# Kernel tuning notes

Hardware: AMD Instinct MI355X
Metric: run time of the kernel (lower is better)

The kernel has to match this reference:

```python
import jax, jax.numpy as jnp
import numpy as np

N_IN = 512    # samples per input window
N_VP = 12     # number of weighted Hermite basis functions
BATCH = 65536


def ada_weighted_hermite(n_in, n_vp, params):
    """Adaptive weighted Hermite system (VPNet-style).

    params = [dilation, translation].
    Returns phi [n_in, n_vp], dphi [n_in, 2*n_vp] (d/d dilation cols then
    d/d translation cols), ind [2, 2*n_vp] (row 0: basis index, row 1: param index).
    """
    dilation, translation = params[0], params[1]
    t = jnp.arange(n_in, dtype=params.dtype) - (n_in - 1) / 2.0  # centered grid
    xs = dilation * (t - translation)  # [n_in]
    pi14 = jnp.pi ** -0.25
    phi0 = pi14 * jnp.exp(-0.5 * xs * xs)
    phis = [phi0]
    if n_vp > 1:
        phis.append(jnp.sqrt(2.0) * xs * phi0)
    for k in range(2, n_vp):
        phis.append(jnp.sqrt(2.0 / k) * xs * phis[k - 1]
                    - jnp.sqrt((k - 1) / k) * phis[k - 2])
    phi = jnp.stack(phis, axis=1)  # [n_in, n_vp]
    # d phi_k / d xs = sqrt(2k) phi_{k-1} - xs * phi_k
    dphis = [-xs * phis[0]]
    for k in range(1, n_vp):
        dphis.append(jnp.sqrt(2.0 * k) * phis[k - 1] - xs * phis[k])
    dphi_dx = jnp.stack(dphis, axis=1)  # [n_in, n_vp]
    d_dil = dphi_dx * (t - translation)[:, None]   # chain rule: dxs/d dilation
    d_tr = -dilation * dphi_dx                     # dxs/d translation
    dphi = jnp.concatenate([d_dil, d_tr], axis=1)  # [n_in, 2*n_vp]
    ind = jnp.stack([jnp.tile(jnp.arange(n_vp), 2),
                     jnp.repeat(jnp.arange(2), n_vp)])  # [2, 2*n_vp]
    return phi, dphi, ind


def setup_inputs() -> dict:
    key = jax.random.key(0)
    kx, _ = jax.random.split(key)
    x = jax.random.normal(kx, (BATCH, N_IN), dtype=jnp.float32)
    w = jnp.array([0.1, 0.0], dtype=jnp.float32)  # [dilation, translation]
    return {"x": x, "w": w}


def reference(x, w):
    phi, dphi, ind = ada_weighted_hermite(N_IN, N_VP, w)
    phip = jnp.linalg.pinv(phi, rcond=1e-15)      # [n_vp, n_in]
    coeffs = phip @ x.T                           # [n_vp, batch]
    return coeffs.T                               # [batch, n_vp]
```

## Files before the change

kernel.cpp:

```cpp
#include <hip/hip_runtime.h>

#define N_IN 512
#define N_VP 12
#define BATCH 65536

#define SPLIT 4
#define ROWS 64
#define CPW (N_IN / SPLIT)
#define CHUNK 16
#define NCHW (CPW / CHUNK)

__global__ __launch_bounds__(512) void build_W_kernel(const float* __restrict__ w,
                                                      float* __restrict__ Wg) {
    __shared__ float sphiT[N_VP][N_IN];
    __shared__ float Gp[2][N_VP][N_VP];
    __shared__ float G[N_VP][N_VP], Y[N_VP][N_VP], T[N_VP][N_VP];

    const int tid = threadIdx.x;
    const float dil = w[0];
    const float tr  = w[1];

    float ph[N_VP];
    {
        const float t  = (float)tid - 0.5f * (float)(N_IN - 1);
        const float xs = dil * (t - tr);
        ph[0] = 0.7511255444649425f * expf(-0.5f * xs * xs);
        ph[1] = 1.4142135623730951f * xs * ph[0];
#pragma unroll
        for (int k = 2; k < N_VP; ++k)
            ph[k] = sqrtf(2.0f / (float)k) * xs * ph[k - 1]
                  - sqrtf((float)(k - 1) / (float)k) * ph[k - 2];
#pragma unroll
        for (int k = 0; k < N_VP; ++k) sphiT[k][tid] = ph[k];
    }
    __syncthreads();

    if (tid < 288) {
        const int p = tid >> 1;
        const int i = p / N_VP, j = p % N_VP;
        const int m0 = (tid & 1) * 256;
        const float4* __restrict__ pi = reinterpret_cast<const float4*>(&sphiT[i][m0]);
        const float4* __restrict__ pj = reinterpret_cast<const float4*>(&sphiT[j][m0]);
        float s = 0.0f;
#pragma unroll 4
        for (int q = 0; q < 64; ++q) {
            const float4 a = pi[q], b = pj[q];
            s += a.x * b.x + a.y * b.y + a.z * b.z + a.w * b.w;
        }
        Gp[tid & 1][i][j] = s;
    }
    __syncthreads();
    const int ii = (tid < 144) ? tid / N_VP : 0;
    const int jj = (tid < 144) ? tid % N_VP : 0;
    if (tid < 144) {
        G[ii][jj] = Gp[0][ii][jj] + Gp[1][ii][jj];
        Y[ii][jj] = (ii == jj) ? dil : 0.0f;
    }
    __syncthreads();

    for (int it = 0; it < 3; ++it) {
        if (tid < 144) {
            float s = 0.0f;
#pragma unroll
            for (int k = 0; k < N_VP; ++k) s += G[ii][k] * Y[k][jj];
            T[ii][jj] = s;
        }
        __syncthreads();
        float v = 0.0f;
        if (tid < 144) {
            float s = 0.0f;
#pragma unroll
            for (int k = 0; k < N_VP; ++k) s += Y[ii][k] * T[k][jj];
            v = 2.0f * Y[ii][jj] - s;
        }
        __syncthreads();
        if (tid < 144) Y[ii][jj] = v;
        __syncthreads();
    }

#pragma unroll
    for (int k = 0; k < N_VP; ++k) {
        float s = 0.0f;
#pragma unroll
        for (int j2 = 0; j2 < N_VP; ++j2) s += Y[k][j2] * ph[j2];
        Wg[tid * N_VP + k] = s;
    }
}

__device__ __forceinline__ void load_chunk(const float* __restrict__ xq,
                                           const int off[4], int c, float4 pre[4]) {
#pragma unroll
    for (int i = 0; i < 4; ++i)
        pre[i] = *reinterpret_cast<const float4*>(xq + off[i] + c * CHUNK);
}

__device__ __forceinline__ void store_chunk(float4* __restrict__ dst, int lane,
                                            const float4 pre[4]) {
#pragma unroll
    for (int i = 0; i < 4; ++i) dst[i * 64 + lane] = pre[i];
}

__device__ __forceinline__ void compute_chunk(const float4* __restrict__ buf,
                                              int lane, int qx,
                                              const float* __restrict__ wb,
                                              float acc[N_VP]) {
#pragma unroll
    for (int q = 0; q < 4; ++q) {
        const float4 xv = buf[(lane << 2) + (q ^ qx)];
        const float* __restrict__ w4 = wb + q * (4 * N_VP);
#pragma unroll
        for (int k = 0; k < N_VP; ++k) acc[k] = fmaf(xv.x, w4[k], acc[k]);
#pragma unroll
        for (int k = 0; k < N_VP; ++k) acc[k] = fmaf(xv.y, w4[N_VP + k], acc[k]);
#pragma unroll
        for (int k = 0; k < N_VP; ++k) acc[k] = fmaf(xv.z, w4[2 * N_VP + k], acc[k]);
#pragma unroll
        for (int k = 0; k < N_VP; ++k) acc[k] = fmaf(xv.w, w4[3 * N_VP + k], acc[k]);
    }
}

__global__ __launch_bounds__(256, 4) void coeffs_kernel(const float* __restrict__ x,
                                                        const float* __restrict__ Wg,
                                                        float* __restrict__ out) {
    __shared__ float4 sb[SPLIT][2][256];
    const int tid  = threadIdx.x;
    const int lane = tid & 63;
    const int s    = __builtin_amdgcn_readfirstlane(tid >> 6);
    const int qx   = (lane >> 1) & 3;
    const size_t rowbase = (size_t)blockIdx.x * ROWS;
    const float* __restrict__ xq = x + rowbase * N_IN + (size_t)s * CPW;
    const float* __restrict__ wbase = Wg + s * CPW * N_VP;

    int off[4];
#pragma unroll
    for (int i = 0; i < 4; ++i) {
        const int f = i * 64 + lane, t = f >> 2, q0 = f & 3;
        const int qg = q0 ^ ((t >> 1) & 3);
        off[i] = t * N_IN + qg * 4;
    }

    float4 preA[4], preB[4];
    load_chunk(xq, off, 0, preA);
    load_chunk(xq, off, 1, preB);
    store_chunk(&sb[s][0][0], lane, preA);

    float acc[N_VP];
#pragma unroll
    for (int k = 0; k < N_VP; ++k) acc[k] = 0.0f;

#pragma unroll
    for (int c = 0; c < NCHW; ++c) {
        if (c + 1 < NCHW) store_chunk(&sb[s][(c + 1) & 1][0], lane,
                                      (c & 1) ? preA : preB);
        if (c + 2 < NCHW) load_chunk(xq, off, c + 2,
                                     (c & 1) ? preB : preA);
        compute_chunk(&sb[s][c & 1][0], lane, qx, wbase + c * (CHUNK * N_VP), acc);
    }

    __syncthreads();
    float4* part4 = reinterpret_cast<float4*>(&sb[0][0][0]);
    part4[s * 192 + lane * 3 + 0] = make_float4(acc[0], acc[1], acc[2],  acc[3]);
    part4[s * 192 + lane * 3 + 1] = make_float4(acc[4], acc[5], acc[6],  acc[7]);
    part4[s * 192 + lane * 3 + 2] = make_float4(acc[8], acc[9], acc[10], acc[11]);
    __syncthreads();
    if (tid < 192) {
        const float4 v0 = part4[tid], v1 = part4[192 + tid];
        const float4 v2 = part4[384 + tid], v3 = part4[576 + tid];
        float4 r;
        r.x = (v0.x + v1.x) + (v2.x + v3.x);
        r.y = (v0.y + v1.y) + (v2.y + v3.y);
        r.z = (v0.z + v1.z) + (v2.z + v3.z);
        r.w = (v0.w + v1.w) + (v2.w + v3.w);
        reinterpret_cast<float4*>(out + rowbase * N_VP)[tid] = r;
    }
}

extern "C" void kernel_launch(void* const* d_in, const int* in_sizes, int n_in,
                              void* d_out, int out_size, void* d_ws, size_t ws_size,
                              hipStream_t stream) {
    const float* x  = (const float*)d_in[0];
    const float* w  = (const float*)d_in[1];
    float* out      = (float*)d_out;
    float* Wg       = (float*)d_ws;

    build_W_kernel<<<1, 512, 0, stream>>>(w, Wg);
    coeffs_kernel<<<BATCH / ROWS, 256, 0, stream>>>(x, Wg, out);
}
```

Before: 42.88 us.

## Stream x chunks directly into LDS with global_load_lds and manual waitcnt

Replaces the register-staged double buffer (global load into VGPRs, then LDS store) with asynchronous global_load_lds transfers that write straight into shared memory. Explicit vmcnt and lgkmcnt waits plus sched_barriers order each chunk's arrival, its read into registers, and the issue of the chunk two steps ahead. The occupancy hint of 4 blocks per CU is also dropped from launch_bounds. This removes the staging VGPRs and the LDS store instructions, but relies on hand-counted wait counts, which are fragile if the compiler emits other memory operations such as the W loads.

```diff
diff --git a/kernel.cpp b/kernel.cpp
--- a/kernel.cpp
+++ b/kernel.cpp
@@ -9,6 +9,9 @@
 #define CPW (N_IN / SPLIT)
 #define CHUNK 16
 #define NCHW (CPW / CHUNK)
+
+#define GLB_CAST(p) ((const __attribute__((address_space(1))) unsigned int*)(p))
+#define LDS_CAST(p) ((__attribute__((address_space(3))) unsigned int*)(p))
 
 __global__ __launch_bounds__(512) void build_W_kernel(const float* __restrict__ w,
                                                       float* __restrict__ Wg) {
@@ -87,41 +90,9 @@
     }
 }
 
-__device__ __forceinline__ void load_chunk(const float* __restrict__ xq,
-                                           const int off[4], int c, float4 pre[4]) {
-#pragma unroll
-    for (int i = 0; i < 4; ++i)
-        pre[i] = *reinterpret_cast<const float4*>(xq + off[i] + c * CHUNK);
-}
-
-__device__ __forceinline__ void store_chunk(float4* __restrict__ dst, int lane,
-                                            const float4 pre[4]) {
-#pragma unroll
-    for (int i = 0; i < 4; ++i) dst[i * 64 + lane] = pre[i];
-}
-
-__device__ __forceinline__ void compute_chunk(const float4* __restrict__ buf,
-                                              int lane, int qx,
-                                              const float* __restrict__ wb,
-                                              float acc[N_VP]) {
-#pragma unroll
-    for (int q = 0; q < 4; ++q) {
-        const float4 xv = buf[(lane << 2) + (q ^ qx)];
-        const float* __restrict__ w4 = wb + q * (4 * N_VP);
-#pragma unroll
-        for (int k = 0; k < N_VP; ++k) acc[k] = fmaf(xv.x, w4[k], acc[k]);
-#pragma unroll
-        for (int k = 0; k < N_VP; ++k) acc[k] = fmaf(xv.y, w4[N_VP + k], acc[k]);
-#pragma unroll
-        for (int k = 0; k < N_VP; ++k) acc[k] = fmaf(xv.z, w4[2 * N_VP + k], acc[k]);
-#pragma unroll
-        for (int k = 0; k < N_VP; ++k) acc[k] = fmaf(xv.w, w4[3 * N_VP + k], acc[k]);
-    }
-}
-
-__global__ __launch_bounds__(256, 4) void coeffs_kernel(const float* __restrict__ x,
-                                                        const float* __restrict__ Wg,
-                                                        float* __restrict__ out) {
+__global__ __launch_bounds__(256) void coeffs_kernel(const float* __restrict__ x,
+                                                     const float* __restrict__ Wg,
+                                                     float* __restrict__ out) {
     __shared__ float4 sb[SPLIT][2][256];
     const int tid  = threadIdx.x;
     const int lane = tid & 63;
@@ -139,10 +110,17 @@
         off[i] = t * N_IN + qg * 4;
     }
 
-    float4 preA[4], preB[4];
-    load_chunk(xq, off, 0, preA);
-    load_chunk(xq, off, 1, preB);
-    store_chunk(&sb[s][0][0], lane, preA);
+#define ISSUE_CHUNK(c)                                                         \
+    {                                                                          \
+        float4* dst_ = &sb[s][(c) & 1][0];                                     \
+        _Pragma("unroll")                                                      \
+        for (int i_ = 0; i_ < 4; ++i_)                                         \
+            __builtin_amdgcn_global_load_lds(GLB_CAST(xq + off[i_] + (c) * CHUNK), \
+                                             LDS_CAST(dst_ + i_ * 64), 16, 0, 0); \
+    }
+
+    ISSUE_CHUNK(0)
+    ISSUE_CHUNK(1)
 
     float acc[N_VP];
 #pragma unroll
@@ -150,11 +128,32 @@
 
 #pragma unroll
     for (int c = 0; c < NCHW; ++c) {
-        if (c + 1 < NCHW) store_chunk(&sb[s][(c + 1) & 1][0], lane,
-                                      (c & 1) ? preA : preB);
-        if (c + 2 < NCHW) load_chunk(xq, off, c + 2,
-                                     (c & 1) ? preB : preA);
-        compute_chunk(&sb[s][c & 1][0], lane, qx, wbase + c * (CHUNK * N_VP), acc);
+        if (c < NCHW - 1) asm volatile("s_waitcnt vmcnt(4)" ::: "memory");
+        else              asm volatile("s_waitcnt vmcnt(0)" ::: "memory");
+        __builtin_amdgcn_sched_barrier(0);
+
+        const float4* __restrict__ buf = &sb[s][c & 1][0];
+        float4 xv[4];
+#pragma unroll
+        for (int q = 0; q < 4; ++q) xv[q] = buf[(lane << 2) + (q ^ qx)];
+
+        asm volatile("s_waitcnt lgkmcnt(0)" ::: "memory");
+        __builtin_amdgcn_sched_barrier(0);
+        if (c + 2 < NCHW) ISSUE_CHUNK(c + 2)
+
+        const float* __restrict__ wb = wbase + c * (CHUNK * N_VP);
+#pragma unroll
+        for (int q = 0; q < 4; ++q) {
+            const float* __restrict__ w4 = wb + q * (4 * N_VP);
+#pragma unroll
+            for (int k = 0; k < N_VP; ++k) acc[k] = fmaf(xv[q].x, w4[k], acc[k]);
+#pragma unroll
+            for (int k = 0; k < N_VP; ++k) acc[k] = fmaf(xv[q].y, w4[N_VP + k], acc[k]);
+#pragma unroll
+            for (int k = 0; k < N_VP; ++k) acc[k] = fmaf(xv[q].z, w4[2 * N_VP + k], acc[k]);
+#pragma unroll
+            for (int k = 0; k < N_VP; ++k) acc[k] = fmaf(xv[q].w, w4[3 * N_VP + k], acc[k]);
+        }
     }
 
     __syncthreads();
```

Result: slower. 46.77 us (+9.1%).

## Widen coalesced row loads and use single swizzled LDS buffer per wave

Applied to the files above, without the earlier changes.

Doubles the per-wave chunk width to 32 floats. Each row is now fetched by 8 lanes as a contiguous 128-byte segment, where before 4 lanes fetched 64 bytes. The per-wave double-buffered LDS staging is replaced by one XOR-swizzled row-major buffer, written after the compute on the current chunk, with two register prefetch sets of 8 float4 each. The aim is better global-memory coalescing and fewer load instructions per byte on this bandwidth-bound projection. The cost is higher register pressure and a serialized compute-then-store order inside each wave.

```diff
diff --git a/kernel.cpp b/kernel.cpp
--- a/kernel.cpp
+++ b/kernel.cpp
@@ -4,10 +4,10 @@
 #define N_VP 12
 #define BATCH 65536
 
-#define SPLIT 4
+#define WAVES 4
 #define ROWS 64
-#define CPW (N_IN / SPLIT)
-#define CHUNK 16
+#define CPW (N_IN / WAVES)
+#define CHUNK 32
 #define NCHW (CPW / CHUNK)
 
 __global__ __launch_bounds__(512) void build_W_kernel(const float* __restrict__ w,
@@ -87,62 +87,44 @@
     }
 }
 
-__device__ __forceinline__ void load_chunk(const float* __restrict__ xq,
-                                           const int off[4], int c, float4 pre[4]) {
-#pragma unroll
-    for (int i = 0; i < 4; ++i)
-        pre[i] = *reinterpret_cast<const float4*>(xq + off[i] + c * CHUNK);
-}
-
-__device__ __forceinline__ void store_chunk(float4* __restrict__ dst, int lane,
-                                            const float4 pre[4]) {
-#pragma unroll
-    for (int i = 0; i < 4; ++i) dst[i * 64 + lane] = pre[i];
-}
-
-__device__ __forceinline__ void compute_chunk(const float4* __restrict__ buf,
-                                              int lane, int qx,
-                                              const float* __restrict__ wb,
-                                              float acc[N_VP]) {
-#pragma unroll
-    for (int q = 0; q < 4; ++q) {
-        const float4 xv = buf[(lane << 2) + (q ^ qx)];
-        const float* __restrict__ w4 = wb + q * (4 * N_VP);
-#pragma unroll
-        for (int k = 0; k < N_VP; ++k) acc[k] = fmaf(xv.x, w4[k], acc[k]);
-#pragma unroll
-        for (int k = 0; k < N_VP; ++k) acc[k] = fmaf(xv.y, w4[N_VP + k], acc[k]);
-#pragma unroll
-        for (int k = 0; k < N_VP; ++k) acc[k] = fmaf(xv.z, w4[2 * N_VP + k], acc[k]);
-#pragma unroll
-        for (int k = 0; k < N_VP; ++k) acc[k] = fmaf(xv.w, w4[3 * N_VP + k], acc[k]);
-    }
-}
-
 __global__ __launch_bounds__(256, 4) void coeffs_kernel(const float* __restrict__ x,
                                                         const float* __restrict__ Wg,
                                                         float* __restrict__ out) {
-    __shared__ float4 sb[SPLIT][2][256];
+    __shared__ float sb[WAVES][ROWS][CHUNK];
     const int tid  = threadIdx.x;
     const int lane = tid & 63;
     const int s    = __builtin_amdgcn_readfirstlane(tid >> 6);
-    const int qx   = (lane >> 1) & 3;
     const size_t rowbase = (size_t)blockIdx.x * ROWS;
-    const float* __restrict__ xq = x + rowbase * N_IN + (size_t)s * CPW;
+    const float* __restrict__ xq = x + rowbase * N_IN + s * CPW;
     const float* __restrict__ wbase = Wg + s * CPW * N_VP;
 
-    int off[4];
+    const int t0 = lane >> 3, q0 = lane & 7;
+    const int gbase = t0 * N_IN + q0 * 4;
+    float* const wr0 = &sb[s][0][0] + t0 * CHUNK + ((q0 ^ (t0 & 7)) << 2);
+
+    const float* rd[8];
 #pragma unroll
-    for (int i = 0; i < 4; ++i) {
-        const int f = i * 64 + lane, t = f >> 2, q0 = f & 3;
-        const int qg = q0 ^ ((t >> 1) & 3);
-        off[i] = t * N_IN + qg * 4;
+    for (int g = 0; g < 8; ++g)
+        rd[g] = &sb[s][lane][(g ^ (lane & 7)) << 2];
+
+#define LOADC(c, pre)                                                          \
+    {                                                                          \
+        _Pragma("unroll")                                                      \
+        for (int i_ = 0; i_ < 8; ++i_)                                         \
+            pre[i_] = *reinterpret_cast<const float4*>(                        \
+                xq + gbase + i_ * 8 * N_IN + (c) * CHUNK);                     \
+    }
+#define STOREC(pre)                                                            \
+    {                                                                          \
+        _Pragma("unroll")                                                      \
+        for (int i_ = 0; i_ < 8; ++i_)                                         \
+            *reinterpret_cast<float4*>(wr0 + i_ * 8 * CHUNK) = pre[i_];        \
     }
 
-    float4 preA[4], preB[4];
-    load_chunk(xq, off, 0, preA);
-    load_chunk(xq, off, 1, preB);
-    store_chunk(&sb[s][0][0], lane, preA);
+    float4 preA[8], preB[8];
+    LOADC(0, preA)
+    STOREC(preA)
+    LOADC(1, preB)
 
     float acc[N_VP];
 #pragma unroll
@@ -150,11 +132,26 @@
 
 #pragma unroll
     for (int c = 0; c < NCHW; ++c) {
-        if (c + 1 < NCHW) store_chunk(&sb[s][(c + 1) & 1][0], lane,
-                                      (c & 1) ? preA : preB);
-        if (c + 2 < NCHW) load_chunk(xq, off, c + 2,
-                                     (c & 1) ? preB : preA);
-        compute_chunk(&sb[s][c & 1][0], lane, qx, wbase + c * (CHUNK * N_VP), acc);
+        const float* __restrict__ wc = wbase + c * (CHUNK * N_VP);
+#pragma unroll
+        for (int g = 0; g < 8; ++g) {
+            const float4 xv = *reinterpret_cast<const float4*>(rd[g]);
+            const float* __restrict__ w4 = wc + g * (4 * N_VP);
+#pragma unroll
+            for (int k = 0; k < N_VP; ++k) acc[k] = fmaf(xv.x, w4[k], acc[k]);
+#pragma unroll
+            for (int k = 0; k < N_VP; ++k) acc[k] = fmaf(xv.y, w4[N_VP + k], acc[k]);
+#pragma unroll
+            for (int k = 0; k < N_VP; ++k) acc[k] = fmaf(xv.z, w4[2 * N_VP + k], acc[k]);
+#pragma unroll
+            for (int k = 0; k < N_VP; ++k) acc[k] = fmaf(xv.w, w4[3 * N_VP + k], acc[k]);
+        }
+        if (c + 1 < NCHW) {
+            if (c & 1) { STOREC(preA) } else { STOREC(preB) }
+        }
+        if (c + 2 < NCHW) {
+            if (c & 1) { LOADC(c + 2, preB) } else { LOADC(c + 2, preA) }
+        }
     }
 
     __syncthreads();
```

Result: no change. 43.45 us (+1.3%).

## Fuse projection-matrix build into coeffs kernel, computing W per block in LDS

Applied to the files above, without the earlier changes.

Removes the separate single-block build_W kernel and has each of the 1024 blocks recompute the Hermite basis, a symmetric Gram matrix (only the upper triangle), three Newton-Schulz iterations and the projection matrix W in LDS, before the streaming GEMV. This drops one kernel launch and the serial dependency on a one-block kernel, and W is read from LDS instead of global memory. The cost is redundant per-block setup with several syncthreads, 24KB of extra LDS per block that may lower occupancy, and a simpler single-buffered staging pipeline for x.

```diff
diff --git a/kernel.cpp b/kernel.cpp
--- a/kernel.cpp
+++ b/kernel.cpp
@@ -4,132 +4,24 @@
 #define N_VP 12
 #define BATCH 65536
 
-#define SPLIT 4
+#define WAVES 4
 #define ROWS 64
-#define CPW (N_IN / SPLIT)
+#define CPW (N_IN / WAVES)
 #define CHUNK 16
 #define NCHW (CPW / CHUNK)
 
-__global__ __launch_bounds__(512) void build_W_kernel(const float* __restrict__ w,
-                                                      float* __restrict__ Wg) {
-    __shared__ float sphiT[N_VP][N_IN];
-    __shared__ float Gp[2][N_VP][N_VP];
-    __shared__ float G[N_VP][N_VP], Y[N_VP][N_VP], T[N_VP][N_VP];
+__global__ __launch_bounds__(256, 4) void vp_fused_kernel(const float* __restrict__ x,
+                                                          const float* __restrict__ w,
+                                                          float* __restrict__ out) {
+    __shared__ float wlds[N_IN * N_VP];
+    __shared__ float stage[WAVES * ROWS * CHUNK];
 
-    const int tid = threadIdx.x;
-    const float dil = w[0];
-    const float tr  = w[1];
-
-    float ph[N_VP];
-    {
-        const float t  = (float)tid - 0.5f * (float)(N_IN - 1);
-        const float xs = dil * (t - tr);
-        ph[0] = 0.7511255444649425f * expf(-0.5f * xs * xs);
-        ph[1] = 1.4142135623730951f * xs * ph[0];
-#pragma unroll
-        for (int k = 2; k < N_VP; ++k)
-            ph[k] = sqrtf(2.0f / (float)k) * xs * ph[k - 1]
-                  - sqrtf((float)(k - 1) / (float)k) * ph[k - 2];
-#pragma unroll
-        for (int k = 0; k < N_VP; ++k) sphiT[k][tid] = ph[k];
-    }
-    __syncthreads();
-
-    if (tid < 288) {
-        const int p = tid >> 1;
-        const int i = p / N_VP, j = p % N_VP;
-        const int m0 = (tid & 1) * 256;
-        const float4* __restrict__ pi = reinterpret_cast<const float4*>(&sphiT[i][m0]);
-        const float4* __restrict__ pj = reinterpret_cast<const float4*>(&sphiT[j][m0]);
-        float s = 0.0f;
-#pragma unroll 4
-        for (int q = 0; q < 64; ++q) {
-            const float4 a = pi[q], b = pj[q];
-            s += a.x * b.x + a.y * b.y + a.z * b.z + a.w * b.w;
-        }
-        Gp[tid & 1][i][j] = s;
-    }
-    __syncthreads();
-    const int ii = (tid < 144) ? tid / N_VP : 0;
-    const int jj = (tid < 144) ? tid % N_VP : 0;
-    if (tid < 144) {
-        G[ii][jj] = Gp[0][ii][jj] + Gp[1][ii][jj];
-        Y[ii][jj] = (ii == jj) ? dil : 0.0f;
-    }
-    __syncthreads();
-
-    for (int it = 0; it < 3; ++it) {
-        if (tid < 144) {
-            float s = 0.0f;
-#pragma unroll
-            for (int k = 0; k < N_VP; ++k) s += G[ii][k] * Y[k][jj];
-            T[ii][jj] = s;
-        }
-        __syncthreads();
-        float v = 0.0f;
-        if (tid < 144) {
-            float s = 0.0f;
-#pragma unroll
-            for (int k = 0; k < N_VP; ++k) s += Y[ii][k] * T[k][jj];
-            v = 2.0f * Y[ii][jj] - s;
-        }
-        __syncthreads();
-        if (tid < 144) Y[ii][jj] = v;
-        __syncthreads();
-    }
-
-#pragma unroll
-    for (int k = 0; k < N_VP; ++k) {
-        float s = 0.0f;
-#pragma unroll
-        for (int j2 = 0; j2 < N_VP; ++j2) s += Y[k][j2] * ph[j2];
-        Wg[tid * N_VP + k] = s;
-    }
-}
-
-__device__ __forceinline__ void load_chunk(const float* __restrict__ xq,
-                                           const int off[4], int c, float4 pre[4]) {
-#pragma unroll
-    for (int i = 0; i < 4; ++i)
-        pre[i] = *reinterpret_cast<const float4*>(xq + off[i] + c * CHUNK);
-}
-
-__device__ __forceinline__ void store_chunk(float4* __restrict__ dst, int lane,
-                                            const float4 pre[4]) {
-#pragma unroll
-    for (int i = 0; i < 4; ++i) dst[i * 64 + lane] = pre[i];
-}
-
-__device__ __forceinline__ void compute_chunk(const float4* __restrict__ buf,
-                                              int lane, int qx,
-                                              const float* __restrict__ wb,
-                                              float acc[N_VP]) {
-#pragma unroll
-    for (int q = 0; q < 4; ++q) {
-        const float4 xv = buf[(lane << 2) + (q ^ qx)];
-        const float* __restrict__ w4 = wb + q * (4 * N_VP);
-#pragma unroll
-        for (int k = 0; k < N_VP; ++k) acc[k] = fmaf(xv.x, w4[k], acc[k]);
-#pragma unroll
-        for (int k = 0; k < N_VP; ++k) acc[k] = fmaf(xv.y, w4[N_VP + k], acc[k]);
-#pragma unroll
-        for (int k = 0; k < N_VP; ++k) acc[k] = fmaf(xv.z, w4[2 * N_VP + k], acc[k]);
-#pragma unroll
-        for (int k = 0; k < N_VP; ++k) acc[k] = fmaf(xv.w, w4[3 * N_VP + k], acc[k]);
-    }
-}
-
-__global__ __launch_bounds__(256, 4) void coeffs_kernel(const float* __restrict__ x,
-                                                        const float* __restrict__ Wg,
-                                                        float* __restrict__ out) {
-    __shared__ float4 sb[SPLIT][2][256];
     const int tid  = threadIdx.x;
     const int lane = tid & 63;
     const int s    = __builtin_amdgcn_readfirstlane(tid >> 6);
     const int qx   = (lane >> 1) & 3;
     const size_t rowbase = (size_t)blockIdx.x * ROWS;
-    const float* __restrict__ xq = x + rowbase * N_IN + (size_t)s * CPW;
-    const float* __restrict__ wbase = Wg + s * CPW * N_VP;
+    const float* __restrict__ xq = x + rowbase * N_IN + s * CPW;
 
     int off[4];
 #pragma unroll
@@ -139,10 +31,113 @@
         off[i] = t * N_IN + qg * 4;
     }
 
-    float4 preA[4], preB[4];
-    load_chunk(xq, off, 0, preA);
-    load_chunk(xq, off, 1, preB);
-    store_chunk(&sb[s][0][0], lane, preA);
+    float4 pre[4];
+#pragma unroll
+    for (int i = 0; i < 4; ++i)
+        pre[i] = *reinterpret_cast<const float4*>(xq + off[i]);
+
+    const float dil = w[0];
+    const float tr  = w[1];
+
+#pragma unroll
+    for (int half = 0; half < 2; ++half) {
+        const int n = tid + half * 256;
+        const float t  = (float)n - 0.5f * (float)(N_IN - 1);
+        const float xs = dil * (t - tr);
+        float pm2 = 0.7511255444649425f * expf(-0.5f * xs * xs);
+        float pm1 = 1.4142135623730951f * xs * pm2;
+        wlds[0 * N_IN + n] = pm2;
+        wlds[1 * N_IN + n] = pm1;
+#pragma unroll
+        for (int k = 2; k < N_VP; ++k) {
+            const float pk = sqrtf(2.0f / (float)k) * xs * pm1
+                           - sqrtf((float)(k - 1) / (float)k) * pm2;
+            wlds[k * N_IN + n] = pk;
+            pm2 = pm1; pm1 = pk;
+        }
+    }
+    __syncthreads();
+
+    float* const Gp = stage;
+    float* const G  = stage + 160;
+    float* const Y  = stage + 304;
+    float* const T  = stage + 448;
+
+    if (tid < 156) {
+        const int p = tid >> 1, h = tid & 1;
+        int i = 0, rem = p;
+        while (rem >= N_VP - i) { rem -= N_VP - i; ++i; }
+        const int j = i + rem;
+        const float4* __restrict__ pi =
+            reinterpret_cast<const float4*>(wlds + i * N_IN + h * 256);
+        const float4* __restrict__ pj =
+            reinterpret_cast<const float4*>(wlds + j * N_IN + h * 256);
+        float acc = 0.0f;
+#pragma unroll 4
+        for (int q = 0; q < 64; ++q) {
+            const float4 a = pi[q], b = pj[q];
+            acc += a.x * b.x + a.y * b.y + a.z * b.z + a.w * b.w;
+        }
+        Gp[h * 78 + p] = acc;
+    }
+    __syncthreads();
+    if (tid < 78) {
+        int i = 0, rem = tid;
+        while (rem >= N_VP - i) { rem -= N_VP - i; ++i; }
+        const int j = i + rem;
+        const float v = Gp[tid] + Gp[78 + tid];
+        G[i * N_VP + j] = v;
+        G[j * N_VP + i] = v;
+    }
+    if (tid < 144) {
+        const int ii = tid / N_VP, jj = tid % N_VP;
+        Y[tid] = (ii == jj) ? dil : 0.0f;
+    }
+    __syncthreads();
+
+    for (int it = 0; it < 3; ++it) {
+        if (tid < 144) {
+            const int ii = tid / N_VP, jj = tid % N_VP;
+            float sa = 0.0f;
+#pragma unroll
+            for (int k = 0; k < N_VP; ++k) sa += G[ii * N_VP + k] * Y[k * N_VP + jj];
+            T[tid] = sa;
+        }
+        __syncthreads();
+        float v = 0.0f;
+        if (tid < 144) {
+            const int ii = tid / N_VP, jj = tid % N_VP;
+            float sa = 0.0f;
+#pragma unroll
+            for (int k = 0; k < N_VP; ++k) sa += Y[ii * N_VP + k] * T[k * N_VP + jj];
+            v = 2.0f * Y[tid] - sa;
+        }
+        __syncthreads();
+        if (tid < 144) Y[tid] = v;
+        __syncthreads();
+    }
+
+    float w0[N_VP], w1[N_VP];
+#pragma unroll
+    for (int k = 0; k < N_VP; ++k) {
+        float s0 = 0.0f, s1 = 0.0f;
+#pragma unroll
+        for (int j = 0; j < N_VP; ++j) {
+            const float yk = Y[k * N_VP + j];
+            s0 += yk * wlds[j * N_IN + tid];
+            s1 += yk * wlds[j * N_IN + tid + 256];
+        }
+        w0[k] = s0; w1[k] = s1;
+    }
+    __syncthreads();
+#pragma unroll
+    for (int k = 0; k < N_VP; ++k) {
+        wlds[tid * N_VP + k]         = w0[k];
+        wlds[(tid + 256) * N_VP + k] = w1[k];
+    }
+    __syncthreads();
+
+    float4* const sb4 = reinterpret_cast<float4*>(stage + s * (ROWS * CHUNK));
 
     float acc[N_VP];
 #pragma unroll
@@ -150,21 +145,37 @@
 
 #pragma unroll
     for (int c = 0; c < NCHW; ++c) {
-        if (c + 1 < NCHW) store_chunk(&sb[s][(c + 1) & 1][0], lane,
-                                      (c & 1) ? preA : preB);
-        if (c + 2 < NCHW) load_chunk(xq, off, c + 2,
-                                     (c & 1) ? preB : preA);
-        compute_chunk(&sb[s][c & 1][0], lane, qx, wbase + c * (CHUNK * N_VP), acc);
+#pragma unroll
+        for (int i = 0; i < 4; ++i) sb4[i * 64 + lane] = pre[i];
+        if (c + 1 < NCHW) {
+#pragma unroll
+            for (int i = 0; i < 4; ++i)
+                pre[i] = *reinterpret_cast<const float4*>(xq + off[i] + (c + 1) * CHUNK);
+        }
+        const float* __restrict__ wc = wlds + (s * CPW + c * CHUNK) * N_VP;
+#pragma unroll
+        for (int q = 0; q < 4; ++q) {
+            const float4 xv = sb4[(lane << 2) + (q ^ qx)];
+            const float* __restrict__ w4 = wc + q * (4 * N_VP);
+#pragma unroll
+            for (int k = 0; k < N_VP; ++k) acc[k] = fmaf(xv.x, w4[k], acc[k]);
+#pragma unroll
+            for (int k = 0; k < N_VP; ++k) acc[k] = fmaf(xv.y, w4[N_VP + k], acc[k]);
+#pragma unroll
+            for (int k = 0; k < N_VP; ++k) acc[k] = fmaf(xv.z, w4[2 * N_VP + k], acc[k]);
+#pragma unroll
+            for (int k = 0; k < N_VP; ++k) acc[k] = fmaf(xv.w, w4[3 * N_VP + k], acc[k]);
+        }
     }
 
     __syncthreads();
-    float4* part4 = reinterpret_cast<float4*>(&sb[0][0][0]);
+    float4* part4 = reinterpret_cast<float4*>(stage);
     part4[s * 192 + lane * 3 + 0] = make_float4(acc[0], acc[1], acc[2],  acc[3]);
     part4[s * 192 + lane * 3 + 1] = make_float4(acc[4], acc[5], acc[6],  acc[7]);
     part4[s * 192 + lane * 3 + 2] = make_float4(acc[8], acc[9], acc[10], acc[11]);
     __syncthreads();
     if (tid < 192) {
-        const float4 v0 = part4[tid], v1 = part4[192 + tid];
+        const float4 v0 = part4[tid],       v1 = part4[192 + tid];
         const float4 v2 = part4[384 + tid], v3 = part4[576 + tid];
         float4 r;
         r.x = (v0.x + v1.x) + (v2.x + v3.x);
@@ -181,8 +192,6 @@
     const float* x  = (const float*)d_in[0];
     const float* w  = (const float*)d_in[1];
     float* out      = (float*)d_out;
-    float* Wg       = (float*)d_ws;
 
-    build_W_kernel<<<1, 512, 0, stream>>>(w, Wg);
-    coeffs_kernel<<<BATCH / ROWS, 256, 0, stream>>>(x, Wg, out);
+    vp_fused_kernel<<<BATCH / ROWS, 256, 0, stream>>>(x, w, out);
 }
```

New measurement: 99.23 us. +131.4%, slower.
